# Kernel optimization log

Hardware: AMD Instinct MI355X
Metric: run time of the kernel (lower is better)

The kernel has to match this reference:

```python
import jax, jax.numpy as jnp
import numpy as np

M, N, T = 10, 10, 2048
H1 = (M + N) * 10 * 8          # 1600, first linear width
HID = (M * M + N * N) * 10     # 2000, GRU hidden dim
H2 = M * N * 1 * 4             # 400, second linear width


def setup_inputs() -> dict:
    key = jax.random.key(0)
    ks = jax.random.split(key, 16)
    rn = lambda k, shp, s=1.0: jax.random.normal(k, shp, dtype=jnp.float32) * s
    f = rn(ks[0], (M, M))
    f = 0.95 * f / jnp.linalg.norm(f, ord=2)  # stable state-transition matrix
    return {
        "y": rn(ks[2], (N, T)),
        "f": f,
        "h": rn(ks[1], (N, M), 1.0 / np.sqrt(M)),
        "m1x_0": rn(ks[3], (M,)),
        "hn0": rn(ks[4], (HID,)),
        "W1": rn(ks[5], (H1, M + N), 1.0 / np.sqrt(M + N)),
        "b1": rn(ks[6], (H1,), 0.01),
        "W_ih": rn(ks[7], (3 * HID, H1), 1.0 / np.sqrt(H1)),
        "W_hh": rn(ks[8], (3 * HID, HID), 1.0 / np.sqrt(HID)),
        "b_ih": rn(ks[9], (3 * HID,), 0.01),
        "b_hh": rn(ks[10], (3 * HID,), 0.01),
        "W2": rn(ks[11], (H2, HID), 1.0 / np.sqrt(HID)),
        "b2": rn(ks[12], (H2,), 0.01),
        "W3": rn(ks[13], (M * N, H2), 0.01 / np.sqrt(H2)),
        "b3": rn(ks[14], (M * N,), 0.001),
    }


def _l2norm(v, eps=1e-12):
    # torch func.normalize(v, p=2, dim=0): v / max(||v||, eps)
    return v / jnp.maximum(jnp.linalg.norm(v), eps)


def _kalmannet_forward(y, f, h, m1x_0, hn0, W1, b1, W_ih, W_hh, b_ih, b_hh, W2, b2, W3, b3):
    m, n = f.shape[0], h.shape[0]
    hid = W_hh.shape[1]

    def step(carry, yt):
        post, prior_prev, hn = carry
        # _step_prior
        prior = f @ post            # m1x_prior = f @ m1x_posterior
        m1y = h @ prior             # predicted observation
        # _step_k_gain_est: two L2-normalized difference features
        dm1y = _l2norm(yt - m1y)
        dm1x = _l2norm(post - prior_prev)
        x_in = jnp.concatenate([dm1y, dm1x])       # [n + m]
        # _k_gain_step: Linear -> ReLU -> single-step GRU -> Linear -> ReLU -> Linear
        a1 = jax.nn.relu(W1 @ x_in + b1)           # [H1]
        gi = W_ih @ a1 + b_ih                      # [3*hid]
        gh = W_hh @ hn + b_hh                      # [3*hid]
        r = jax.nn.sigmoid(gi[:hid] + gh[:hid])
        z = jax.nn.sigmoid(gi[hid:2 * hid] + gh[hid:2 * hid])
        ng = jnp.tanh(gi[2 * hid:] + r * gh[2 * hid:])
        hn_new = (1.0 - z) * ng + z * hn           # torch GRU cell update
        a2 = jax.nn.relu(W2 @ hn_new + b2)         # [H2]
        k_gain = (W3 @ a2 + b3).reshape(m, n)      # Kalman gain [m, n]
        # innovation update
        post_new = prior + k_gain @ (yt - m1y)
        return (post_new, prior, hn_new), post_new

    _, xs = jax.lax.scan(step, (m1x_0, m1x_0, hn0), y.T)  # scan over T
    return xs.T  # [m, T]


def reference(y, f, h, m1x_0, hn0, W1, b1, W_ih, W_hh, b_ih, b_hh, W2, b2, W3, b3):
    return _kalmannet_forward(y, f, h, m1x_0, hn0, W1, b1, W_ih, W_hh, b_ih, b_hh, W2, b2, W3, b3)
```

## Files before the change

kernel.cpp:

```cpp
#include <hip/hip_runtime.h>
#include <math.h>


#define T_STEPS 2048
#define H1      1600
#define HID     2000
#define NBLK    250
#define NTHR    512
#define DPAD    64
#define RMAGIC  0x1357u

struct Params {
  const float *y, *f, *h, *m1x0, *hn0, *W1, *b1, *Wih, *Whh, *bih, *bhh, *W2, *b2, *W3, *b3;
  float* out;
  float* w3t;
  float* hn_g;
  float* delta;
  unsigned* bar;
};

__device__ __forceinline__ float dot4(float4 w, float4 x, float acc) {
  acc = fmaf(w.x, x.x, acc); acc = fmaf(w.y, x.y, acc);
  acc = fmaf(w.z, x.z, acc); acc = fmaf(w.w, x.w, acc);
  return acc;
}

__device__ __forceinline__ float wave_reduce(float v) {
#pragma unroll
  for (int o = 32; o > 0; o >>= 1) v += __shfl_xor(v, o, 64);
  return v;
}

__device__ __forceinline__ float sigm(float x) { return 1.0f / (1.0f + expf(-x)); }

__device__ __forceinline__ void gbar(unsigned* cnt, unsigned* gen) {
  __syncthreads();
  if (threadIdx.x == 0) {
    __threadfence();
    unsigned g = __hip_atomic_load(gen, __ATOMIC_RELAXED, __HIP_MEMORY_SCOPE_AGENT);
    unsigned prev = __hip_atomic_fetch_add(cnt, 1u, __ATOMIC_RELAXED, __HIP_MEMORY_SCOPE_AGENT);
    if (prev == NBLK - 1) {
      __hip_atomic_store(cnt, 0u, __ATOMIC_RELAXED, __HIP_MEMORY_SCOPE_AGENT);
      __threadfence();
      __hip_atomic_store(gen, g + 1u, __ATOMIC_RELAXED, __HIP_MEMORY_SCOPE_AGENT);
    } else {
      while (__hip_atomic_load(gen, __ATOMIC_RELAXED, __HIP_MEMORY_SCOPE_AGENT) == g)
        __builtin_amdgcn_s_sleep(1);
    }
    __threadfence();
  }
  __syncthreads();
}

__global__ __launch_bounds__(NTHR, 2) void knet_kernel(Params p) {
  const int tid  = threadIdx.x;
  const int blk  = blockIdx.x;
  const int wv   = tid >> 6;
  const int lane = tid & 63;

  __shared__ __align__(16) float a1_lds[1792];
  __shared__ __align__(16) float hn_lds[2048];
  __shared__ float f_lds[100], h_lds[100], b3_lds[100];
  __shared__ float xin_lds[20];
  __shared__ float post_lds[10], prpv_lds[10], prior_lds[10], innov_lds[10];
  __shared__ float a2part_lds[8];
  __shared__ float a2_lds[2], b2_lds[2];

  if (tid < 100) { f_lds[tid] = p.f[tid]; h_lds[tid] = p.h[tid]; b3_lds[tid] = p.b3[tid]; }
  if (tid < 10)  { post_lds[tid] = p.m1x0[tid]; prpv_lds[tid] = p.m1x0[tid]; }
  if (tid < 500) ((float4*)hn_lds)[tid] = ((const float4*)p.hn0)[tid];
  if (tid < 48)  hn_lds[2000 + tid] = 0.f;
  if (tid < 192) a1_lds[1600 + tid] = 0.f;

  const int u = blk * 8 + wv;
  float4 wih[3][7];
  float4 whh[3][8];
  const float4 z4 = make_float4(0.f, 0.f, 0.f, 0.f);
#pragma unroll
  for (int g = 0; g < 3; ++g) {
    const float4* rw = (const float4*)(p.Wih + (size_t)(g * HID + u) * H1);
#pragma unroll
    for (int j = 0; j < 7; ++j) {
      int fi = lane + 64 * j;
      wih[g][j] = (fi < 400) ? rw[fi] : z4;
    }
    const float4* rv = (const float4*)(p.Whh + (size_t)(g * HID + u) * HID);
#pragma unroll
    for (int j = 0; j < 8; ++j) {
      int fi = lane + 64 * j;
      whh[g][j] = (fi < 500) ? rv[fi] : z4;
    }
  }
  const float bihr = p.bih[u], bihz = p.bih[HID + u], bihn = p.bih[2 * HID + u];
  const float bhhr = p.bhh[u], bhhz = p.bhh[HID + u], bhhn = p.bhh[2 * HID + u];

  const int w2row = blk * 2 + (wv >> 2);
  const int w2c   = wv & 3;
  float4 w2r[2];
  w2r[0] = z4; w2r[1] = z4;
  if (blk < 200) {
    const float4* rw2 = (const float4*)(p.W2 + (size_t)w2row * HID);
#pragma unroll
    for (int k = 0; k < 2; ++k) {
      int fi = w2c * 125 + lane + 64 * k;
      if (lane + 64 * k < 125) w2r[k] = rw2[fi];
    }
    if (tid < 2) b2_lds[tid] = p.b2[blk * 2 + tid];
    if (tid < 100) {
      int s0 = blk * 2, s1 = blk * 2 + 1;
      p.w3t[s0 * 100 + tid] = p.W3[tid * 400 + s0];
      p.w3t[s1 * 100 + tid] = p.W3[tid * 400 + s1];
    }
  }

  if (blk == 0) {
    for (int i = tid; i < 2 * 10 * DPAD; i += NTHR) p.delta[i] = 0.f;
    __syncthreads();
    if (tid == 0) {
      __hip_atomic_store(p.bar + 0,  0u, __ATOMIC_RELAXED, __HIP_MEMORY_SCOPE_AGENT);
      __hip_atomic_store(p.bar + 32, 0u, __ATOMIC_RELAXED, __HIP_MEMORY_SCOPE_AGENT);
      __threadfence();
      __hip_atomic_store(p.bar + 64, RMAGIC, __ATOMIC_RELAXED, __HIP_MEMORY_SCOPE_AGENT);
    }
  } else {
    if (tid == 0) {
      while (__hip_atomic_load(p.bar + 64, __ATOMIC_RELAXED, __HIP_MEMORY_SCOPE_AGENT) != RMAGIC)
        __builtin_amdgcn_s_sleep(1);
      __threadfence();
    }
  }
  __syncthreads();

  for (int t = 0; t <= T_STEPS; ++t) {
    if (wv == 0) {
      const bool act = lane < 10;
      if (t > 0) {
        float pr_old = act ? prior_lds[lane] : 0.f;
        float dsum   = act ? p.delta[((t - 1) & 1) * 10 * DPAD + lane * DPAD] : 0.f;
        float b3f = 0.f;
        if (act) {
#pragma unroll
          for (int c = 0; c < 10; ++c) b3f = fmaf(innov_lds[c], b3_lds[lane * 10 + c], b3f);
        }
        float postn = pr_old + dsum + b3f;
        if (act) {
          prpv_lds[lane] = pr_old;
          post_lds[lane] = postn;
          if (blk == 0) p.out[lane * T_STEPS + (t - 1)] = postn;
        }
      }
      if (t < T_STEPS) {
        float pr = 0.f;
        if (act) {
#pragma unroll
          for (int j = 0; j < 10; ++j) pr = fmaf(f_lds[lane * 10 + j], post_lds[j], pr);
          prior_lds[lane] = pr;
        }
        float m1y = 0.f;
#pragma unroll
        for (int j = 0; j < 10; ++j) {
          float prj = __shfl(pr, j, 64);
          if (act) m1y = fmaf(h_lds[lane * 10 + j], prj, m1y);
        }
        float yv  = act ? p.y[lane * T_STEPS + t] : 0.f;
        float inn = act ? (yv - m1y) : 0.f;
        float s1 = inn * inn;
#pragma unroll
        for (int o = 8; o > 0; o >>= 1) s1 += __shfl_xor(s1, o, 16);
        float dm1y = inn / fmaxf(sqrtf(s1), 1e-12f);
        float dx = act ? (post_lds[lane] - prpv_lds[lane]) : 0.f;
        float s2 = dx * dx;
#pragma unroll
        for (int o = 8; o > 0; o >>= 1) s2 += __shfl_xor(s2, o, 16);
        float dm1x = dx / fmaxf(sqrtf(s2), 1e-12f);
        if (act) {
          xin_lds[lane]      = dm1y;
          xin_lds[10 + lane] = dm1x;
          innov_lds[lane]    = inn;
        }
      }
    }
    if (t == T_STEPS) break;
    __syncthreads();

#pragma unroll
    for (int k = 0; k < 4; ++k) {
      int r = tid + NTHR * k;
      if (r < H1) {
        const float4* w1r = (const float4*)(p.W1 + (size_t)r * 20);
        float acc = p.b1[r];
#pragma unroll
        for (int q = 0; q < 5; ++q) {
          float4 w = w1r[q];
          acc = fmaf(w.x, xin_lds[q * 4 + 0], acc);
          acc = fmaf(w.y, xin_lds[q * 4 + 1], acc);
          acc = fmaf(w.z, xin_lds[q * 4 + 2], acc);
          acc = fmaf(w.w, xin_lds[q * 4 + 3], acc);
        }
        a1_lds[r] = fmaxf(acc, 0.f);
      }
    }
    __syncthreads();

    {
      const float4* a1v = (const float4*)a1_lds;
      const float4* hnv = (const float4*)hn_lds;
      float gr = 0.f, gz = 0.f, gn = 0.f;
#pragma unroll
      for (int j = 0; j < 7; ++j) {
        float4 x = a1v[lane + 64 * j];
        gr = dot4(wih[0][j], x, gr);
        gz = dot4(wih[1][j], x, gz);
        gn = dot4(wih[2][j], x, gn);
      }
      float hr = 0.f, hz = 0.f, hg = 0.f;
#pragma unroll
      for (int j = 0; j < 8; ++j) {
        float4 x = hnv[lane + 64 * j];
        hr = dot4(whh[0][j], x, hr);
        hz = dot4(whh[1][j], x, hz);
        hg = dot4(whh[2][j], x, hg);
      }
      gr = wave_reduce(gr); gz = wave_reduce(gz); gn = wave_reduce(gn);
      hr = wave_reduce(hr); hz = wave_reduce(hz); hg = wave_reduce(hg);
      float rg = sigm(gr + bihr + hr + bhhr);
      float zg = sigm(gz + bihz + hz + bhhz);
      float ng = tanhf(gn + bihn + rg * (hg + bhhn));
      float hnew = (1.f - zg) * ng + zg * hn_lds[u];
      if (lane == 0) p.hn_g[(t & 1) * HID + u] = hnew;
    }
    gbar(p.bar + 0, p.bar + 32);

    {
      const int par = t & 1;
      if (tid < 500)
        ((float4*)hn_lds)[tid] = ((const float4*)(p.hn_g + par * HID))[tid];
      __syncthreads();
      if (blk < 200) {
        const float4* hnv = (const float4*)hn_lds;
        float acc = 0.f;
#pragma unroll
        for (int k = 0; k < 2; ++k)
          acc = dot4(w2r[k], hnv[w2c * 125 + lane + 64 * k], acc);
        acc = wave_reduce(acc);
        if (lane == 0) a2part_lds[wv] = acc;
      }
      __syncthreads();
      if (blk < 200) {
        if (tid < 2)
          a2_lds[tid] = fmaxf(a2part_lds[tid * 4] + a2part_lds[tid * 4 + 1] +
                              a2part_lds[tid * 4 + 2] + a2part_lds[tid * 4 + 3] +
                              b2_lds[tid], 0.f);
      }
      __syncthreads();
      if (blk < 200 && wv == 0 && lane < 20) {
        int q = lane / 10, col = lane % 10;
        int row = blk * 2 + q;
        float mr = 0.f;
#pragma unroll
        for (int c = 0; c < 10; ++c)
          mr = fmaf(innov_lds[c], p.w3t[row * 100 + col * 10 + c], mr);
        float v = a2_lds[q] * mr;
        float v2 = __shfl(v, lane + 10, 64);
        if (lane < 10)
          atomicAdd(&p.delta[par * 10 * DPAD + lane * DPAD], v + v2);
      }
      if (blk == 0)
        for (int i = tid; i < 10 * DPAD; i += NTHR) p.delta[(par ^ 1) * 10 * DPAD + i] = 0.f;
    }
    gbar(p.bar + 0, p.bar + 32);
  }
}

extern "C" void kernel_launch(void* const* d_in, const int* in_sizes, int n_in,
                              void* d_out, int out_size, void* d_ws, size_t ws_size,
                              hipStream_t stream) {
  Params p;
  p.y    = (const float*)d_in[0];
  p.f    = (const float*)d_in[1];
  p.h    = (const float*)d_in[2];
  p.m1x0 = (const float*)d_in[3];
  p.hn0  = (const float*)d_in[4];
  p.W1   = (const float*)d_in[5];
  p.b1   = (const float*)d_in[6];
  p.Wih  = (const float*)d_in[7];
  p.Whh  = (const float*)d_in[8];
  p.bih  = (const float*)d_in[9];
  p.bhh  = (const float*)d_in[10];
  p.W2   = (const float*)d_in[11];
  p.b2   = (const float*)d_in[12];
  p.W3   = (const float*)d_in[13];
  p.b3   = (const float*)d_in[14];
  p.out  = (float*)d_out;

  float* ws = (float*)d_ws;
  p.w3t   = ws;
  p.hn_g  = ws + 40000;
  p.delta = ws + 44000;
  p.bar   = (unsigned*)(ws + 45312);

  void* args[] = { &p };
  hipLaunchCooperativeKernel((const void*)knet_kernel, dim3(NBLK), dim3(NTHR),
                             args, 0, stream);
}
```

Measured before the change: 53.95 ms.

## Split each GRU unit across two waves with 1024-thread blocks and spread delta atomics

Blocks grow to 1024 threads, and each GRU hidden unit is now computed by two waves, each handling half of the W_ih and W_hh row. Partial sums are combined through shared memory, which halves per-thread register weight storage and shortens the per-wave dot-product chain. The W3 transpose moves from global workspace into LDS, and W2 is read straight from global each step instead of being held in registers. The delta accumulators are spread over 8 slots selected by block index to reduce atomic contention, at the cost of an extra __syncthreads and a few more loads per step.

```diff
diff --git a/kernel.cpp b/kernel.cpp
--- a/kernel.cpp
+++ b/kernel.cpp
@@ -6,14 +6,12 @@
 #define H1      1600
 #define HID     2000
 #define NBLK    250
-#define NTHR    512
-#define DPAD    64
+#define NTHR    1024
 #define RMAGIC  0x1357u
 
 struct Params {
   const float *y, *f, *h, *m1x0, *hn0, *W1, *b1, *Wih, *Whh, *bih, *bhh, *W2, *b2, *W3, *b3;
   float* out;
-  float* w3t;
   float* hn_g;
   float* delta;
   unsigned* bar;
@@ -52,69 +50,63 @@
   __syncthreads();
 }
 
-__global__ __launch_bounds__(NTHR, 2) void knet_kernel(Params p) {
+__global__ __launch_bounds__(NTHR, 4) void knet_kernel(Params p) {
   const int tid  = threadIdx.x;
   const int blk  = blockIdx.x;
   const int wv   = tid >> 6;
   const int lane = tid & 63;
-
-  __shared__ __align__(16) float a1_lds[1792];
+  const int u    = blk * 8 + (wv >> 1);
+  const int half = wv & 1;
+
+  __shared__ __align__(16) float a1_lds[1856];
   __shared__ __align__(16) float hn_lds[2048];
   __shared__ float f_lds[100], h_lds[100], b3_lds[100];
+  __shared__ float w3t_lds[200];
   __shared__ float xin_lds[20];
   __shared__ float post_lds[10], prpv_lds[10], prior_lds[10], innov_lds[10];
-  __shared__ float a2part_lds[8];
+  __shared__ float gpart_lds[16][4];
+  __shared__ float a2part_lds[16];
   __shared__ float a2_lds[2], b2_lds[2];
+  __shared__ float bih_l[24], bhh_l[24];
 
   if (tid < 100) { f_lds[tid] = p.f[tid]; h_lds[tid] = p.h[tid]; b3_lds[tid] = p.b3[tid]; }
   if (tid < 10)  { post_lds[tid] = p.m1x0[tid]; prpv_lds[tid] = p.m1x0[tid]; }
   if (tid < 500) ((float4*)hn_lds)[tid] = ((const float4*)p.hn0)[tid];
   if (tid < 48)  hn_lds[2000 + tid] = 0.f;
-  if (tid < 192) a1_lds[1600 + tid] = 0.f;
-
-  const int u = blk * 8 + wv;
-  float4 wih[3][7];
-  float4 whh[3][8];
+  if (tid < 256) a1_lds[1600 + tid] = 0.f;
+  if (tid < 24) {
+    bih_l[tid] = p.bih[(tid >> 3) * HID + blk * 8 + (tid & 7)];
+    bhh_l[tid] = p.bhh[(tid >> 3) * HID + blk * 8 + (tid & 7)];
+  }
+  if (blk < 200) {
+    if (tid < 2) b2_lds[tid] = p.b2[blk * 2 + tid];
+    if (tid < 200) {
+      int q = tid / 100, i = tid % 100;
+      w3t_lds[tid] = p.W3[i * 400 + blk * 2 + q];
+    }
+  }
+
+  float4 wih[3][4];
+  float4 whh[3][4];
   const float4 z4 = make_float4(0.f, 0.f, 0.f, 0.f);
 #pragma unroll
   for (int g = 0; g < 3; ++g) {
-    const float4* rw = (const float4*)(p.Wih + (size_t)(g * HID + u) * H1);
-#pragma unroll
-    for (int j = 0; j < 7; ++j) {
+    const float4* rw = (const float4*)(p.Wih + (size_t)(g * HID + u) * H1) + half * 200;
+#pragma unroll
+    for (int j = 0; j < 4; ++j) {
       int fi = lane + 64 * j;
-      wih[g][j] = (fi < 400) ? rw[fi] : z4;
-    }
-    const float4* rv = (const float4*)(p.Whh + (size_t)(g * HID + u) * HID);
-#pragma unroll
-    for (int j = 0; j < 8; ++j) {
+      wih[g][j] = (fi < 200) ? rw[fi] : z4;
+    }
+    const float4* rv = (const float4*)(p.Whh + (size_t)(g * HID + u) * HID) + half * 250;
+#pragma unroll
+    for (int j = 0; j < 4; ++j) {
       int fi = lane + 64 * j;
-      whh[g][j] = (fi < 500) ? rv[fi] : z4;
-    }
-  }
-  const float bihr = p.bih[u], bihz = p.bih[HID + u], bihn = p.bih[2 * HID + u];
-  const float bhhr = p.bhh[u], bhhz = p.bhh[HID + u], bhhn = p.bhh[2 * HID + u];
-
-  const int w2row = blk * 2 + (wv >> 2);
-  const int w2c   = wv & 3;
-  float4 w2r[2];
-  w2r[0] = z4; w2r[1] = z4;
-  if (blk < 200) {
-    const float4* rw2 = (const float4*)(p.W2 + (size_t)w2row * HID);
-#pragma unroll
-    for (int k = 0; k < 2; ++k) {
-      int fi = w2c * 125 + lane + 64 * k;
-      if (lane + 64 * k < 125) w2r[k] = rw2[fi];
-    }
-    if (tid < 2) b2_lds[tid] = p.b2[blk * 2 + tid];
-    if (tid < 100) {
-      int s0 = blk * 2, s1 = blk * 2 + 1;
-      p.w3t[s0 * 100 + tid] = p.W3[tid * 400 + s0];
-      p.w3t[s1 * 100 + tid] = p.W3[tid * 400 + s1];
+      whh[g][j] = (fi < 250) ? rv[fi] : z4;
     }
   }
 
   if (blk == 0) {
-    for (int i = tid; i < 2 * 10 * DPAD; i += NTHR) p.delta[i] = 0.f;
+    for (int i = tid; i < 2 * 8 * 160; i += NTHR) p.delta[i] = 0.f;
     __syncthreads();
     if (tid == 0) {
       __hip_atomic_store(p.bar + 0,  0u, __ATOMIC_RELAXED, __HIP_MEMORY_SCOPE_AGENT);
@@ -136,7 +128,12 @@
       const bool act = lane < 10;
       if (t > 0) {
         float pr_old = act ? prior_lds[lane] : 0.f;
-        float dsum   = act ? p.delta[((t - 1) & 1) * 10 * DPAD + lane * DPAD] : 0.f;
+        float dsum = 0.f;
+        if (act) {
+          const float* dbase = p.delta + ((t - 1) & 1) * 1280 + lane * 16;
+#pragma unroll
+          for (int c = 0; c < 8; ++c) dsum += dbase[c * 160];
+        }
         float b3f = 0.f;
         if (act) {
 #pragma unroll
@@ -184,7 +181,7 @@
     __syncthreads();
 
 #pragma unroll
-    for (int k = 0; k < 4; ++k) {
+    for (int k = 0; k < 2; ++k) {
       int r = tid + NTHR * k;
       if (r < H1) {
         const float4* w1r = (const float4*)(p.W1 + (size_t)r * 20);
@@ -203,31 +200,45 @@
     __syncthreads();
 
     {
-      const float4* a1v = (const float4*)a1_lds;
-      const float4* hnv = (const float4*)hn_lds;
-      float gr = 0.f, gz = 0.f, gn = 0.f;
-#pragma unroll
-      for (int j = 0; j < 7; ++j) {
+      float s_r = 0.f, s_z = 0.f, s_ni = 0.f, s_nh = 0.f;
+      const float4* a1v = (const float4*)a1_lds + half * 200;
+#pragma unroll
+      for (int j = 0; j < 4; ++j) {
         float4 x = a1v[lane + 64 * j];
-        gr = dot4(wih[0][j], x, gr);
-        gz = dot4(wih[1][j], x, gz);
-        gn = dot4(wih[2][j], x, gn);
-      }
-      float hr = 0.f, hz = 0.f, hg = 0.f;
-#pragma unroll
-      for (int j = 0; j < 8; ++j) {
+        s_r  = dot4(wih[0][j], x, s_r);
+        s_z  = dot4(wih[1][j], x, s_z);
+        s_ni = dot4(wih[2][j], x, s_ni);
+      }
+      const float4* hnv = (const float4*)hn_lds + half * 250;
+#pragma unroll
+      for (int j = 0; j < 4; ++j) {
         float4 x = hnv[lane + 64 * j];
-        hr = dot4(whh[0][j], x, hr);
-        hz = dot4(whh[1][j], x, hz);
-        hg = dot4(whh[2][j], x, hg);
-      }
-      gr = wave_reduce(gr); gz = wave_reduce(gz); gn = wave_reduce(gn);
-      hr = wave_reduce(hr); hz = wave_reduce(hz); hg = wave_reduce(hg);
-      float rg = sigm(gr + bihr + hr + bhhr);
-      float zg = sigm(gz + bihz + hz + bhhz);
-      float ng = tanhf(gn + bihn + rg * (hg + bhhn));
-      float hnew = (1.f - zg) * ng + zg * hn_lds[u];
-      if (lane == 0) p.hn_g[(t & 1) * HID + u] = hnew;
+        s_r  = dot4(whh[0][j], x, s_r);
+        s_z  = dot4(whh[1][j], x, s_z);
+        s_nh = dot4(whh[2][j], x, s_nh);
+      }
+      s_r  = wave_reduce(s_r);
+      s_z  = wave_reduce(s_z);
+      s_ni = wave_reduce(s_ni);
+      s_nh = wave_reduce(s_nh);
+      if (lane == 0) {
+        gpart_lds[wv][0] = s_r;  gpart_lds[wv][1] = s_z;
+        gpart_lds[wv][2] = s_ni; gpart_lds[wv][3] = s_nh;
+      }
+    }
+    __syncthreads();
+    if (tid < 8) {
+      int q = tid;
+      float gr  = gpart_lds[2 * q][0] + gpart_lds[2 * q + 1][0] + bih_l[q]      + bhh_l[q];
+      float gz  = gpart_lds[2 * q][1] + gpart_lds[2 * q + 1][1] + bih_l[8 + q]  + bhh_l[8 + q];
+      float gni = gpart_lds[2 * q][2] + gpart_lds[2 * q + 1][2] + bih_l[16 + q];
+      float gnh = gpart_lds[2 * q][3] + gpart_lds[2 * q + 1][3] + bhh_l[16 + q];
+      float rg = sigm(gr);
+      float zg = sigm(gz);
+      float ng = tanhf(gni + rg * gnh);
+      float hold = hn_lds[blk * 8 + q];
+      float hnew = (1.f - zg) * ng + zg * hold;
+      p.hn_g[(t & 1) * HID + blk * 8 + q] = hnew;
     }
     gbar(p.bar + 0, p.bar + 32);
 
@@ -237,36 +248,38 @@
         ((float4*)hn_lds)[tid] = ((const float4*)(p.hn_g + par * HID))[tid];
       __syncthreads();
       if (blk < 200) {
-        const float4* hnv = (const float4*)hn_lds;
+        const int row = blk * 2 + (wv >> 3);
+        const int c   = wv & 7;
+        const int fi  = c * 64 + lane;
         float acc = 0.f;
-#pragma unroll
-        for (int k = 0; k < 2; ++k)
-          acc = dot4(w2r[k], hnv[w2c * 125 + lane + 64 * k], acc);
+        if (fi < 500) {
+          const float4* w2v = (const float4*)(p.W2 + (size_t)row * HID);
+          acc = dot4(w2v[fi], ((const float4*)hn_lds)[fi], 0.f);
+        }
         acc = wave_reduce(acc);
         if (lane == 0) a2part_lds[wv] = acc;
       }
       __syncthreads();
-      if (blk < 200) {
-        if (tid < 2)
-          a2_lds[tid] = fmaxf(a2part_lds[tid * 4] + a2part_lds[tid * 4 + 1] +
-                              a2part_lds[tid * 4 + 2] + a2part_lds[tid * 4 + 3] +
-                              b2_lds[tid], 0.f);
+      if (blk < 200 && tid < 2) {
+        float s = b2_lds[tid];
+#pragma unroll
+        for (int k = 0; k < 8; ++k) s += a2part_lds[tid * 8 + k];
+        a2_lds[tid] = fmaxf(s, 0.f);
       }
       __syncthreads();
       if (blk < 200 && wv == 0 && lane < 20) {
         int q = lane / 10, col = lane % 10;
-        int row = blk * 2 + q;
         float mr = 0.f;
 #pragma unroll
         for (int c = 0; c < 10; ++c)
-          mr = fmaf(innov_lds[c], p.w3t[row * 100 + col * 10 + c], mr);
+          mr = fmaf(innov_lds[c], w3t_lds[q * 100 + col * 10 + c], mr);
         float v = a2_lds[q] * mr;
         float v2 = __shfl(v, lane + 10, 64);
         if (lane < 10)
-          atomicAdd(&p.delta[par * 10 * DPAD + lane * DPAD], v + v2);
+          atomicAdd(&p.delta[par * 1280 + (blk & 7) * 160 + lane * 16], v + v2);
       }
       if (blk == 0)
-        for (int i = tid; i < 10 * DPAD; i += NTHR) p.delta[(par ^ 1) * 10 * DPAD + i] = 0.f;
+        for (int i = tid; i < 1280; i += NTHR) p.delta[(par ^ 1) * 1280 + i] = 0.f;
     }
     gbar(p.bar + 0, p.bar + 32);
   }
@@ -294,10 +307,9 @@
   p.out  = (float*)d_out;
 
   float* ws = (float*)d_ws;
-  p.w3t   = ws;
-  p.hn_g  = ws + 40000;
-  p.delta = ws + 44000;
-  p.bar   = (unsigned*)(ws + 45312);
+  p.hn_g  = ws;
+  p.delta = ws + 4000;
+  p.bar   = (unsigned*)(ws + 6592);
 
   void* args[] = { &p };
   hipLaunchCooperativeKernel((const void*)knet_kernel, dim3(NBLK), dim3(NTHR),
```

Measured after the change: 67.98 ms. 1.26x slower.
